# Kernel optimization log

Measured on AMD Instinct MI355X. Metric: run time of the kernel, lower is better.

## Reference

```python
import jax, jax.numpy as jnp
import numpy as np

SEQ = 2048
HID = 1024
NH = 16
HD = HID // NH


def setup_inputs() -> dict:
    key = jax.random.key(0)
    ks = jax.random.split(key, 5)
    s = 0.02
    return {
        "hidden_states": jax.random.normal(ks[0], (SEQ, HID), dtype=jnp.float32),
        "w_attn": jax.random.normal(ks[1], (HID, 3 * HID), dtype=jnp.float32) * s,
        "b_attn": jax.random.normal(ks[2], (3 * HID,), dtype=jnp.float32) * s,
        "w_proj": jax.random.normal(ks[3], (HID, HID), dtype=jnp.float32) * s,
        "b_proj": jax.random.normal(ks[4], (HID,), dtype=jnp.float32) * s,
    }


def reference(hidden_states, w_attn, b_attn, w_proj, b_proj):
    S = hidden_states.shape[0]
    qkv = hidden_states @ w_attn + b_attn          # [S, 3H]
    q, k, v = jnp.split(qkv, 3, axis=-1)
    q = q.reshape(S, NH, HD)
    k = k.reshape(S, NH, HD)
    v = v.reshape(S, NH, HD)
    sm_scale = 1.0 / np.sqrt(HD).astype(np.float32)
    # explicit scores [h, q, k] in fp32, as in the torch module
    scores = jnp.einsum('qhd,khd->hqk', q.astype(jnp.float32), k.astype(jnp.float32))
    scores = scores * sm_scale
    causal = jnp.tril(jnp.ones((S, S), dtype=bool))  # [q, k]
    scores = jnp.where(causal[None, :, :], scores, -jnp.inf)
    probs = jax.nn.softmax(scores, axis=-1)
    attn = jnp.einsum('hqk,khd->qhd', probs, v.astype(jnp.float32))  # [S, NH, HD]
    attn = attn.reshape(S, HID).astype(hidden_states.dtype)
    return attn @ w_proj + b_proj
```

## Files before the change

### kernel.cpp

```cpp
#include <hip/hip_runtime.h>
#include <cstdint>
#include <cstddef>

#define SEQ 2048
#define HID 1024
#define NHEAD 16
#define HDIM 64

typedef _Float16 f16;
typedef f16 half8 __attribute__((ext_vector_type(8)));
typedef f16 half4 __attribute__((ext_vector_type(4)));
typedef f16 half2_ __attribute__((ext_vector_type(2)));
typedef float f32x4 __attribute__((ext_vector_type(4)));

#define ASYNC_COPY16(g, l)                                                    \
  __builtin_amdgcn_global_load_lds(                                           \
      (const __attribute__((address_space(1))) void*)(const void*)(g),        \
      (__attribute__((address_space(3))) void*)(void*)(l), 16, 0, 0)

__global__ __launch_bounds__(256) void prologue(
    const float* __restrict__ h, const float* __restrict__ wa,
    const float* __restrict__ wp, f16* __restrict__ h16,
    f16* __restrict__ waT, f16* __restrict__ wpT) {
  const int b = blockIdx.x, tid = threadIdx.x;
  if (b >= 1024) {
    int i = ((b - 1024) * 256 + tid) * 8;
    float4 v0 = *(const float4*)(h + i);
    float4 v1 = *(const float4*)(h + i + 4);
    half8 o;
    o[0] = (f16)v0.x; o[1] = (f16)v0.y; o[2] = (f16)v0.z; o[3] = (f16)v0.w;
    o[4] = (f16)v1.x; o[5] = (f16)v1.y; o[6] = (f16)v1.z; o[7] = (f16)v1.w;
    *(half8*)(h16 + i) = o;
    return;
  }
  const float* src; f16* dst; int C, bx, by;
  if (b < 768) { src = wa; dst = waT; C = 3072; bx = b % 48; by = b / 48; }
  else { int t = b - 768; src = wp; dst = wpT; C = 1024; bx = t & 15; by = t >> 4; }
  __shared__ float tile[64][65];
  const int tx = tid & 63, ty = tid >> 6;
  const int c0 = bx * 64, r0 = by * 64;
#pragma unroll
  for (int i = 0; i < 64; i += 4)
    tile[ty + i][tx] = src[(size_t)(r0 + ty + i) * C + c0 + tx];
  __syncthreads();
#pragma unroll
  for (int i = 0; i < 64; i += 4)
    dst[(size_t)(c0 + ty + i) * 1024 + r0 + tx] = (f16)tile[tx][ty + i];
}

template <int BM, int BN, bool OUT16>
__global__ __launch_bounds__(256) void gemm_f16(
    const f16* __restrict__ A, const f16* __restrict__ Bt,
    const float* __restrict__ bias, void* __restrict__ Cout, int M, int N,
    int K) {
  constexpr int FM = BM / 32, FN = BN / 32;
  __shared__ __align__(16) f16 sA[2][BM * 64];
  __shared__ __align__(16) f16 sB[2][BN * 64];
  const int tid = threadIdx.x;
  const int wave = tid >> 6, lane = tid & 63;
  const int quad = lane >> 4, l16 = lane & 15;
  const int m0 = blockIdx.y * BM, n0 = blockIdx.x * BN;
  const int wm = (wave >> 1) * (BM / 2), wn = (wave & 1) * (BN / 2);
  const int rowA = lane >> 3;
  const int chunkA = (lane & 7) ^ rowA;
  const int r7 = l16 & 7;

  auto stage = [&](int buf, int k0) {
#pragma unroll
    for (int r = wave; r < BM / 8; r += 4)
      ASYNC_COPY16(A + (size_t)(m0 + r * 8 + rowA) * K + k0 + chunkA * 8,
                   &sA[buf][r * 512]);
#pragma unroll
    for (int r = wave; r < BN / 8; r += 4)
      ASYNC_COPY16(Bt + (size_t)(n0 + r * 8 + rowA) * K + k0 + chunkA * 8,
                   &sB[buf][r * 512]);
  };

  f32x4 acc[FM][FN] = {};

  stage(0, 0);
  __syncthreads();
  const int NT = K / 64;
  for (int t = 0; t < NT; ++t) {
    const int cur = t & 1;
    if (t + 1 < NT) stage(cur ^ 1, (t + 1) * 64);

#pragma unroll
    for (int h = 0; h < 2; h++) {
      half8 af[FM], bf[FN];
#pragma unroll
      for (int i = 0; i < FM; i++)
        af[i] = *(const half8*)&sA[cur][(wm + i * 16 + l16) * 64 +
                                        (((h << 2) | quad) ^ r7) * 8];
#pragma unroll
      for (int j = 0; j < FN; j++)
        bf[j] = *(const half8*)&sB[cur][(wn + j * 16 + l16) * 64 +
                                        (((h << 2) | quad) ^ r7) * 8];
#pragma unroll
      for (int i = 0; i < FM; i++)
#pragma unroll
        for (int j = 0; j < FN; j++)
          acc[i][j] = __builtin_amdgcn_mfma_f32_16x16x32_f16(
              af[i], bf[j], acc[i][j], 0, 0, 0);
    }
    __syncthreads();
  }

#pragma unroll
  for (int i = 0; i < FM; i++) {
    int row = m0 + wm + i * 16 + quad * 4;
#pragma unroll
    for (int j = 0; j < FN; j++) {
      int col = n0 + wn + j * 16 + l16;
      float bv = bias[col];
#pragma unroll
      for (int r = 0; r < 4; r++) {
        float v = acc[i][j][r] + bv;
        if (OUT16)
          ((f16*)Cout)[(size_t)(row + r) * N + col] = (f16)v;
        else
          ((float*)Cout)[(size_t)(row + r) * N + col] = v;
      }
    }
  }
}

#define LROW 72
__global__ __launch_bounds__(256, 3) void attn_split(
    const f16* __restrict__ qkv, f16* __restrict__ out,
    f16* __restrict__ Opart, float* __restrict__ ml) {
  const int b = (blockIdx.x & 7) * 80 + (blockIdx.x >> 3);
  const int h = b / 40;
  const int t = b % 40;
  int m, c, nc;
  if (t < 4)       { m = t;                 c = 0;      nc = 1; }
  else if (t < 12) { int u = t - 4;  m = 4 + (u >> 1);  c = u & 1; nc = 2; }
  else if (t < 24) { int u = t - 12; m = 8 + u / 3;     c = u % 3; nc = 3; }
  else             { int u = t - 24; m = 12 + (u >> 2); c = u & 3; nc = 4; }
  const int q0 = m * 128;
  const int T = 2 * m + 2;
  const int kt0 = c * 8;
  const int kt1 = (kt0 + 8 < T) ? kt0 + 8 : T;
  const int maskFrom = 2 * m;

  __shared__ __align__(16) f16 sK[64 * LROW];
  __shared__ __align__(16) f16 sVt[64 * LROW];
  __shared__ __align__(16) f16 sP[4][32 * LROW];

  const int tid = threadIdx.x;
  const int wave = tid >> 6, lane = tid & 63;
  const int quad = lane >> 4, l16 = lane & 15;

  const f16 qs = (f16)0.18033688f;
  half8 qf[2][2];
#pragma unroll
  for (int g = 0; g < 2; g++) {
    const f16* qb = qkv + (size_t)(q0 + wave * 32 + g * 16 + l16) * 3072 +
                    h * HDIM + quad * 8;
    qf[g][0] = *(const half8*)qb;
    qf[g][1] = *(const half8*)(qb + 32);
#pragma unroll
    for (int j = 0; j < 8; j++) { qf[g][0][j] *= qs; qf[g][1][j] *= qs; }
  }

  const f16* kbase = qkv + HID + h * HDIM;
  const f16* vbase = qkv + 2 * HID + h * HDIM;
  const int ks_row = tid >> 3, ks_cc = tid & 7;
  const int vs_d = tid & 63, vs_g = tid >> 6;

  f32x4 o[2][4] = {};
  float m_i[2] = {-1e30f, -1e30f}, l_i[2] = {0.f, 0.f};
  half8 kreg[2], vreg[2];

  auto prefetch = [&](int kt) {
    const int k0 = kt * 64;
#pragma unroll
    for (int i = 0; i < 2; i++) {
      kreg[i] = *(const half8*)(kbase + (size_t)(k0 + ks_row + i * 32) * 3072 +
                                ks_cc * 8);
      half8 col;
#pragma unroll
      for (int j = 0; j < 8; j++)
        col[j] = vbase[(size_t)(k0 + (vs_g + i * 4) * 8 + j) * 3072 + vs_d];
      vreg[i] = col;
    }
  };

  prefetch(kt0);
  for (int kt = kt0; kt < kt1; kt++) {
    const int k0 = kt * 64;
#pragma unroll
    for (int i = 0; i < 2; i++) {
      *(half8*)&sK[(ks_row + i * 32) * LROW + ks_cc * 8] = kreg[i];
      *(half8*)&sVt[vs_d * LROW + (vs_g + i * 4) * 8] = vreg[i];
    }
    __syncthreads();
    if (kt + 1 < kt1) prefetch(kt + 1);

    f32x4 sacc[2][4] = {};
#pragma unroll
    for (int kb = 0; kb < 4; kb++) {
      half8 kf0 = *(const half8*)&sK[(kb * 16 + l16) * LROW + quad * 8];
      half8 kf1 = *(const half8*)&sK[(kb * 16 + l16) * LROW + 32 + quad * 8];
#pragma unroll
      for (int g = 0; g < 2; g++) {
        sacc[g][kb] = __builtin_amdgcn_mfma_f32_16x16x32_f16(kf0, qf[g][0],
                                                             sacc[g][kb], 0, 0, 0);
        sacc[g][kb] = __builtin_amdgcn_mfma_f32_16x16x32_f16(kf1, qf[g][1],
                                                             sacc[g][kb], 0, 0, 0);
      }
    }
    if (kt >= maskFrom) {
#pragma unroll
      for (int g = 0; g < 2; g++) {
        const int qg = q0 + wave * 32 + g * 16 + l16;
#pragma unroll
        for (int kb = 0; kb < 4; kb++) {
          int kg = k0 + kb * 16 + quad * 4;
#pragma unroll
          for (int r = 0; r < 4; r++)
            if (kg + r > qg) sacc[g][kb][r] = -1e30f;
        }
      }
    }
#pragma unroll
    for (int g = 0; g < 2; g++) {
      float mx = -1e30f;
#pragma unroll
      for (int kb = 0; kb < 4; kb++)
#pragma unroll
        for (int r = 0; r < 4; r++) mx = fmaxf(mx, sacc[g][kb][r]);
      mx = fmaxf(mx, __shfl_xor(mx, 16));
      mx = fmaxf(mx, __shfl_xor(mx, 32));
      if (!__all(mx <= m_i[g] + 8.f)) {
        const float mnew = fmaxf(m_i[g], mx);
        const float alpha = exp2f(m_i[g] - mnew);
        l_i[g] *= alpha;
#pragma unroll
        for (int j = 0; j < 4; j++)
#pragma unroll
          for (int r = 0; r < 4; r++) o[g][j][r] *= alpha;
        m_i[g] = mnew;
      }
      float rs = 0.f;
#pragma unroll
      for (int kb = 0; kb < 4; kb++)
#pragma unroll
        for (int r = 0; r < 4; r++) {
          float p = exp2f(sacc[g][kb][r] - m_i[g]);
          sacc[g][kb][r] = p;
          rs += p;
        }
      rs += __shfl_xor(rs, 16);
      rs += __shfl_xor(rs, 32);
      l_i[g] += rs;
      f16* pw = &sP[wave][(g * 16 + l16) * LROW];
#pragma unroll
      for (int kb = 0; kb < 4; kb++) {
        half4 pv;
#pragma unroll
        for (int r = 0; r < 4; r++) pv[r] = (f16)sacc[g][kb][r];
        *(half4*)&pw[kb * 16 + quad * 4] = pv;
      }
    }
    half8 pf[2][2];
#pragma unroll
    for (int g = 0; g < 2; g++) {
      pf[g][0] = *(const half8*)&sP[wave][(g * 16 + l16) * LROW + quad * 8];
      pf[g][1] = *(const half8*)&sP[wave][(g * 16 + l16) * LROW + 32 + quad * 8];
    }
#pragma unroll
    for (int j = 0; j < 4; j++) {
      half8 vf0 = *(const half8*)&sVt[(j * 16 + l16) * LROW + quad * 8];
      half8 vf1 = *(const half8*)&sVt[(j * 16 + l16) * LROW + 32 + quad * 8];
#pragma unroll
      for (int g = 0; g < 2; g++) {
        o[g][j] = __builtin_amdgcn_mfma_f32_16x16x32_f16(vf0, pf[g][0], o[g][j], 0, 0, 0);
        o[g][j] = __builtin_amdgcn_mfma_f32_16x16x32_f16(vf1, pf[g][1], o[g][j], 0, 0, 0);
      }
    }
    __syncthreads();
  }

  if (nc == 1) {
#pragma unroll
    for (int g = 0; g < 2; g++) {
      const float inv = 1.f / l_i[g];
      f16* orow =
          out + (size_t)(q0 + wave * 32 + g * 16 + l16) * HID + h * HDIM;
#pragma unroll
      for (int j = 0; j < 4; j++) {
        half4 hv;
#pragma unroll
        for (int r = 0; r < 4; r++) hv[r] = (f16)(o[g][j][r] * inv);
        *(half4*)&orow[j * 16 + quad * 4] = hv;
      }
    }
  } else {
    int base;
    if (m < 8)       base = (m - 4) * 2;
    else if (m < 12) base = 8 + (m - 8) * 3;
    else             base = 20 + (m - 12) * 4;
    const int slot = h * 36 + base + c;
#pragma unroll
    for (int g = 0; g < 2; g++) {
      const int qrow = wave * 32 + g * 16 + l16;
      f16* op = Opart + (size_t)slot * 8192 + qrow * 64;
#pragma unroll
      for (int j = 0; j < 4; j++) {
        half4 hv;
#pragma unroll
        for (int r = 0; r < 4; r++) hv[r] = (f16)o[g][j][r];
        *(half4*)&op[j * 16 + quad * 4] = hv;
      }
      if (quad == 0) {
        ml[slot * 256 + qrow] = m_i[g];
        ml[slot * 256 + 128 + qrow] = l_i[g];
      }
    }
  }
}

__global__ __launch_bounds__(256) void attn_combine(
    const f16* __restrict__ Opart, const float* __restrict__ ml,
    f16* __restrict__ out) {
  int idx = blockIdx.x * 256 + threadIdx.x;
  int d4 = (idx & 15) * 4;
  int row = (idx >> 4) & 127;
  int rest = idx >> 11;
  int mi = rest % 12;
  int h = rest / 12;
  int m = 4 + mi;
  int nc = (mi < 4) ? 2 : (mi < 8) ? 3 : 4;
  int base = (mi < 4) ? mi * 2 : (mi < 8) ? 8 + (mi - 4) * 3 : 20 + (mi - 8) * 4;
  int slot0 = h * 36 + base;

  float mm[4], ll[4];
  float M = -1e30f;
#pragma unroll
  for (int cc = 0; cc < 4; cc++)
    if (cc < nc) {
      mm[cc] = ml[(slot0 + cc) * 256 + row];
      ll[cc] = ml[(slot0 + cc) * 256 + 128 + row];
      M = fmaxf(M, mm[cc]);
    }
  float L = 0.f, acc[4] = {0.f, 0.f, 0.f, 0.f};
#pragma unroll
  for (int cc = 0; cc < 4; cc++)
    if (cc < nc) {
      float w = exp2f(mm[cc] - M);
      L += w * ll[cc];
      half4 ov = *(const half4*)&Opart[(size_t)(slot0 + cc) * 8192 +
                                       row * 64 + d4];
#pragma unroll
      for (int r = 0; r < 4; r++) acc[r] += w * (float)ov[r];
    }
  const float invL = 1.f / L;
  half4 hv;
#pragma unroll
  for (int r = 0; r < 4; r++) hv[r] = (f16)(acc[r] * invL);
  *(half4*)&out[(size_t)(m * 128 + row) * HID + h * HDIM + d4] = hv;
}

extern "C" void kernel_launch(void* const* d_in, const int* in_sizes, int n_in,
                              void* d_out, int out_size, void* d_ws,
                              size_t ws_size, hipStream_t stream) {
  const float* h = (const float*)d_in[0];
  const float* wa = (const float*)d_in[1];
  const float* ba = (const float*)d_in[2];
  const float* wp = (const float*)d_in[3];
  const float* bp = (const float*)d_in[4];
  float* out = (float*)d_out;

  char* ws = (char*)d_ws;
  f16* h16 = (f16*)(ws);
  f16* waT = (f16*)(ws + (4u << 20));
  f16* wpT = (f16*)(ws + (10u << 20));
  f16* qkv = (f16*)(ws + (12u << 20));
  f16* attn = (f16*)(ws + (24u << 20));
  f16* Opart = (f16*)(ws);
  float* mlbuf = (float*)(ws + 9437184);

  prologue<<<2048, 256, 0, stream>>>(h, wa, wp, h16, waT, wpT);
  gemm_f16<128, 128, true><<<dim3(24, 16), 256, 0, stream>>>(
      h16, waT, ba, qkv, SEQ, 3 * HID, HID);
  attn_split<<<640, 256, 0, stream>>>(qkv, attn, Opart, mlbuf);
  attn_combine<<<1536, 256, 0, stream>>>(Opart, mlbuf, attn);
  gemm_f16<64, 64, false><<<dim3(16, 32), 256, 0, stream>>>(
      attn, wpT, bp, out, SEQ, HID, HID);
}
```

Before: 148.5 us.

## Fuse split-KV attention combine into the output projection GEMM A-loader

Removes the separate attn_combine kernel and the attn buffer. All attention blocks, including single-chunk ones, now write unnormalized partial outputs plus max/sum stats, and the projection GEMM merges those partials while staging its A tiles into shared memory. This saves a kernel launch and one round trip of the attention output through global memory. In exchange, the A tile is loaded synchronously with extra exp math in the GEMM loop instead of by async copy, and the QKV GEMM tile is changed to 64x128.

```diff
diff --git a/kernel.cpp b/kernel.cpp
--- a/kernel.cpp
+++ b/kernel.cpp
@@ -48,10 +48,10 @@
     dst[(size_t)(c0 + ty + i) * 1024 + r0 + tx] = (f16)tile[tx][ty + i];
 }
 
-template <int BM, int BN, bool OUT16>
+template <int BM, int BN>
 __global__ __launch_bounds__(256) void gemm_f16(
     const f16* __restrict__ A, const f16* __restrict__ Bt,
-    const float* __restrict__ bias, void* __restrict__ Cout, int M, int N,
+    const float* __restrict__ bias, f16* __restrict__ Cout, int M, int N,
     int K) {
   constexpr int FM = BM / 32, FN = BN / 32;
   __shared__ __align__(16) f16 sA[2][BM * 64];
@@ -86,16 +86,16 @@
     if (t + 1 < NT) stage(cur ^ 1, (t + 1) * 64);
 
 #pragma unroll
-    for (int h = 0; h < 2; h++) {
+    for (int hh = 0; hh < 2; hh++) {
       half8 af[FM], bf[FN];
 #pragma unroll
       for (int i = 0; i < FM; i++)
         af[i] = *(const half8*)&sA[cur][(wm + i * 16 + l16) * 64 +
-                                        (((h << 2) | quad) ^ r7) * 8];
+                                        (((hh << 2) | quad) ^ r7) * 8];
 #pragma unroll
       for (int j = 0; j < FN; j++)
         bf[j] = *(const half8*)&sB[cur][(wn + j * 16 + l16) * 64 +
-                                        (((h << 2) | quad) ^ r7) * 8];
+                                        (((hh << 2) | quad) ^ r7) * 8];
 #pragma unroll
       for (int i = 0; i < FM; i++)
 #pragma unroll
@@ -114,29 +114,24 @@
       int col = n0 + wn + j * 16 + l16;
       float bv = bias[col];
 #pragma unroll
-      for (int r = 0; r < 4; r++) {
-        float v = acc[i][j][r] + bv;
-        if (OUT16)
-          ((f16*)Cout)[(size_t)(row + r) * N + col] = (f16)v;
-        else
-          ((float*)Cout)[(size_t)(row + r) * N + col] = v;
-      }
+      for (int r = 0; r < 4; r++)
+        Cout[(size_t)(row + r) * N + col] = (f16)(acc[i][j][r] + bv);
     }
   }
 }
 
 #define LROW 72
 __global__ __launch_bounds__(256, 3) void attn_split(
-    const f16* __restrict__ qkv, f16* __restrict__ out,
-    f16* __restrict__ Opart, float* __restrict__ ml) {
+    const f16* __restrict__ qkv, f16* __restrict__ Opart,
+    float* __restrict__ ml) {
   const int b = (blockIdx.x & 7) * 80 + (blockIdx.x >> 3);
   const int h = b / 40;
   const int t = b % 40;
-  int m, c, nc;
-  if (t < 4)       { m = t;                 c = 0;      nc = 1; }
-  else if (t < 12) { int u = t - 4;  m = 4 + (u >> 1);  c = u & 1; nc = 2; }
-  else if (t < 24) { int u = t - 12; m = 8 + u / 3;     c = u % 3; nc = 3; }
-  else             { int u = t - 24; m = 12 + (u >> 2); c = u & 3; nc = 4; }
+  int m, c;
+  if (t < 4)       { m = t;                 c = 0; }
+  else if (t < 12) { int u = t - 4;  m = 4 + (u >> 1);  c = u & 1; }
+  else if (t < 24) { int u = t - 12; m = 8 + u / 3;     c = u % 3; }
+  else             { int u = t - 24; m = 12 + (u >> 2); c = u & 3; }
   const int q0 = m * 128;
   const int T = 2 * m + 2;
   const int kt0 = c * 8;
@@ -282,84 +277,136 @@
     __syncthreads();
   }
 
-  if (nc == 1) {
-#pragma unroll
-    for (int g = 0; g < 2; g++) {
-      const float inv = 1.f / l_i[g];
-      f16* orow =
-          out + (size_t)(q0 + wave * 32 + g * 16 + l16) * HID + h * HDIM;
-#pragma unroll
-      for (int j = 0; j < 4; j++) {
-        half4 hv;
-#pragma unroll
-        for (int r = 0; r < 4; r++) hv[r] = (f16)(o[g][j][r] * inv);
-        *(half4*)&orow[j * 16 + quad * 4] = hv;
-      }
-    }
-  } else {
-    int base;
-    if (m < 8)       base = (m - 4) * 2;
-    else if (m < 12) base = 8 + (m - 8) * 3;
-    else             base = 20 + (m - 12) * 4;
-    const int slot = h * 36 + base + c;
-#pragma unroll
-    for (int g = 0; g < 2; g++) {
-      const int qrow = wave * 32 + g * 16 + l16;
-      f16* op = Opart + (size_t)slot * 8192 + qrow * 64;
-#pragma unroll
-      for (int j = 0; j < 4; j++) {
-        half4 hv;
-#pragma unroll
-        for (int r = 0; r < 4; r++) hv[r] = (f16)o[g][j][r];
-        *(half4*)&op[j * 16 + quad * 4] = hv;
-      }
-      if (quad == 0) {
-        ml[slot * 256 + qrow] = m_i[g];
-        ml[slot * 256 + 128 + qrow] = l_i[g];
-      }
+  int base;
+  if (m < 4)       base = m;
+  else if (m < 8)  base = 4 + (m - 4) * 2;
+  else if (m < 12) base = 12 + (m - 8) * 3;
+  else             base = 24 + (m - 12) * 4;
+  const int slot = h * 40 + base + c;
+#pragma unroll
+  for (int g = 0; g < 2; g++) {
+    const int qrow = wave * 32 + g * 16 + l16;
+    f16* op = Opart + (size_t)slot * 8192 + qrow * 64;
+#pragma unroll
+    for (int j = 0; j < 4; j++) {
+      half4 hv;
+#pragma unroll
+      for (int r = 0; r < 4; r++) hv[r] = (f16)o[g][j][r];
+      *(half4*)&op[j * 16 + quad * 4] = hv;
+    }
+    if (quad == 0) {
+      ml[slot * 256 + qrow] = m_i[g];
+      ml[slot * 256 + 128 + qrow] = l_i[g];
     }
   }
 }
 
-__global__ __launch_bounds__(256) void attn_combine(
+__global__ __launch_bounds__(256) void gemm_proj(
     const f16* __restrict__ Opart, const float* __restrict__ ml,
-    f16* __restrict__ out) {
-  int idx = blockIdx.x * 256 + threadIdx.x;
-  int d4 = (idx & 15) * 4;
-  int row = (idx >> 4) & 127;
-  int rest = idx >> 11;
-  int mi = rest % 12;
-  int h = rest / 12;
-  int m = 4 + mi;
-  int nc = (mi < 4) ? 2 : (mi < 8) ? 3 : 4;
-  int base = (mi < 4) ? mi * 2 : (mi < 8) ? 8 + (mi - 4) * 3 : 20 + (mi - 8) * 4;
-  int slot0 = h * 36 + base;
-
-  float mm[4], ll[4];
-  float M = -1e30f;
-#pragma unroll
-  for (int cc = 0; cc < 4; cc++)
-    if (cc < nc) {
-      mm[cc] = ml[(slot0 + cc) * 256 + row];
-      ll[cc] = ml[(slot0 + cc) * 256 + 128 + row];
-      M = fmaxf(M, mm[cc]);
-    }
-  float L = 0.f, acc[4] = {0.f, 0.f, 0.f, 0.f};
-#pragma unroll
-  for (int cc = 0; cc < 4; cc++)
-    if (cc < nc) {
-      float w = exp2f(mm[cc] - M);
-      L += w * ll[cc];
-      half4 ov = *(const half4*)&Opart[(size_t)(slot0 + cc) * 8192 +
-                                       row * 64 + d4];
-#pragma unroll
-      for (int r = 0; r < 4; r++) acc[r] += w * (float)ov[r];
-    }
-  const float invL = 1.f / L;
-  half4 hv;
-#pragma unroll
-  for (int r = 0; r < 4; r++) hv[r] = (f16)(acc[r] * invL);
-  *(half4*)&out[(size_t)(m * 128 + row) * HID + h * HDIM + d4] = hv;
+    const f16* __restrict__ Bt, const float* __restrict__ bias,
+    float* __restrict__ out) {
+  __shared__ __align__(16) f16 sA[2][64 * 64];
+  __shared__ __align__(16) f16 sB[2][64 * 64];
+  const int tid = threadIdx.x;
+  const int wave = tid >> 6, lane = tid & 63;
+  const int quad = lane >> 4, l16 = lane & 15;
+  const int m0 = blockIdx.y * 64, n0 = blockIdx.x * 64;
+  const int wm = (wave >> 1) * 32, wn = (wave & 1) * 32;
+  const int rowA = lane >> 3;
+  const int chunkA = (lane & 7) ^ rowA;
+  const int r7 = l16 & 7;
+
+  const int mq = m0 >> 7;
+  const int nc = (mq < 4) ? 1 : (mq < 8) ? 2 : (mq < 12) ? 3 : 4;
+  const int base = (mq < 4) ? mq
+                   : (mq < 8) ? 4 + (mq - 4) * 2
+                   : (mq < 12) ? 12 + (mq - 8) * 3
+                   : 24 + (mq - 12) * 4;
+
+  auto stageA = [&](int buf, int t) {
+    const int slot0 = t * 40 + base;
+#pragma unroll
+    for (int rr = 0; rr < 2; rr++) {
+      const int r = wave + rr * 4;
+      const int qrow = (m0 + r * 8 + rowA) & 127;
+      float mm[4], ll[4], M = -1e30f;
+#pragma unroll
+      for (int cc = 0; cc < 4; cc++)
+        if (cc < nc) {
+          mm[cc] = ml[(size_t)(slot0 + cc) * 256 + qrow];
+          ll[cc] = ml[(size_t)(slot0 + cc) * 256 + 128 + qrow];
+          M = fmaxf(M, mm[cc]);
+        }
+      float u[4], L = 0.f;
+#pragma unroll
+      for (int cc = 0; cc < 4; cc++)
+        if (cc < nc) { u[cc] = exp2f(mm[cc] - M); L += u[cc] * ll[cc]; }
+      const float invL = 1.f / L;
+      float a8[8] = {};
+#pragma unroll
+      for (int cc = 0; cc < 4; cc++)
+        if (cc < nc) {
+          half8 v = *(const half8*)&Opart[(size_t)(slot0 + cc) * 8192 +
+                                          qrow * 64 + chunkA * 8];
+          const float uc = u[cc] * invL;
+#pragma unroll
+          for (int j = 0; j < 8; j++) a8[j] += uc * (float)v[j];
+        }
+      half8 o8;
+#pragma unroll
+      for (int j = 0; j < 8; j++) o8[j] = (f16)a8[j];
+      *(half8*)&sA[buf][(r * 8 + rowA) * 64 + (lane & 7) * 8] = o8;
+    }
+  };
+  auto stageB = [&](int buf, int k0) {
+#pragma unroll
+    for (int r = wave; r < 8; r += 4)
+      ASYNC_COPY16(Bt + (size_t)(n0 + r * 8 + rowA) * 1024 + k0 + chunkA * 8,
+                   &sB[buf][r * 512]);
+  };
+
+  f32x4 acc[2][2] = {};
+
+  stageA(0, 0);
+  stageB(0, 0);
+  __syncthreads();
+  for (int t = 0; t < 16; ++t) {
+    const int cur = t & 1;
+    if (t + 1 < 16) { stageA(cur ^ 1, t + 1); stageB(cur ^ 1, (t + 1) * 64); }
+
+#pragma unroll
+    for (int hh = 0; hh < 2; hh++) {
+      half8 af[2], bf[2];
+#pragma unroll
+      for (int i = 0; i < 2; i++)
+        af[i] = *(const half8*)&sA[cur][(wm + i * 16 + l16) * 64 +
+                                        (((hh << 2) | quad) ^ r7) * 8];
+#pragma unroll
+      for (int j = 0; j < 2; j++)
+        bf[j] = *(const half8*)&sB[cur][(wn + j * 16 + l16) * 64 +
+                                        (((hh << 2) | quad) ^ r7) * 8];
+#pragma unroll
+      for (int i = 0; i < 2; i++)
+#pragma unroll
+        for (int j = 0; j < 2; j++)
+          acc[i][j] = __builtin_amdgcn_mfma_f32_16x16x32_f16(
+              af[i], bf[j], acc[i][j], 0, 0, 0);
+    }
+    __syncthreads();
+  }
+
+#pragma unroll
+  for (int i = 0; i < 2; i++) {
+    int row = m0 + wm + i * 16 + quad * 4;
+#pragma unroll
+    for (int j = 0; j < 2; j++) {
+      int col = n0 + wn + j * 16 + l16;
+      float bv = bias[col];
+#pragma unroll
+      for (int r = 0; r < 4; r++)
+        out[(size_t)(row + r) * 1024 + col] = acc[i][j][r] + bv;
+    }
+  }
 }
 
 extern "C" void kernel_launch(void* const* d_in, const int* in_sizes, int n_in,
@@ -375,17 +422,14 @@
   char* ws = (char*)d_ws;
   f16* h16 = (f16*)(ws);
   f16* waT = (f16*)(ws + (4u << 20));
-  f16* wpT = (f16*)(ws + (10u << 20));
   f16* qkv = (f16*)(ws + (12u << 20));
-  f16* attn = (f16*)(ws + (24u << 20));
+  f16* wpT = (f16*)(ws + (32u << 20));
   f16* Opart = (f16*)(ws);
-  float* mlbuf = (float*)(ws + 9437184);
+  float* mlbuf = (float*)(ws + (10u << 20));
 
   prologue<<<2048, 256, 0, stream>>>(h, wa, wp, h16, waT, wpT);
-  gemm_f16<128, 128, true><<<dim3(24, 16), 256, 0, stream>>>(
+  gemm_f16<64, 128><<<dim3(24, 32), 256, 0, stream>>>(
       h16, waT, ba, qkv, SEQ, 3 * HID, HID);
-  attn_split<<<640, 256, 0, stream>>>(qkv, attn, Opart, mlbuf);
-  attn_combine<<<1536, 256, 0, stream>>>(Opart, mlbuf, attn);
-  gemm_f16<64, 64, false><<<dim3(16, 32), 256, 0, stream>>>(
-      attn, wpT, bp, out, SEQ, HID, HID);
+  attn_split<<<640, 256, 0, stream>>>(qkv, Opart, mlbuf);
+  gemm_proj<<<dim3(16, 32), 256, 0, stream>>>(Opart, mlbuf, wpT, bp, out);
 }
```

After: 207.7 us. +39.9%, slower.
